# Kernel optimization log

Hardware: AMD Instinct MI355X
Metric: run time of the kernel (lower is better)

The kernel has to match this reference:

```python
import jax, jax.numpy as jnp
import numpy as np
from jax import lax

NUM_GROUP = 512
GROUP_SIZE = 32


def fps(xyz, npoint):
    """Farthest point sampling. xyz: [B, N, 3] -> centers [B, npoint, 3]."""
    B, N, _ = xyz.shape
    big = jnp.asarray(1e10, xyz.dtype)

    def body(carry, _):
        min_d, farthest = carry  # [B, N], [B]
        centroid = jnp.take_along_axis(xyz, farthest[:, None, None], axis=1)  # [B,1,3]
        d = jnp.sum((xyz - centroid) ** 2, axis=-1)  # [B, N]
        min_d = jnp.minimum(min_d, d)
        nxt = jnp.argmax(min_d, axis=-1).astype(jnp.int32)
        return (min_d, nxt), farthest

    init = (jnp.full((B, N), big, xyz.dtype), jnp.zeros((B,), jnp.int32))
    _, idxs = lax.scan(body, init, None, length=npoint)  # [npoint, B]
    idxs = idxs.T  # [B, npoint]
    return jnp.take_along_axis(xyz, idxs[..., None], axis=1)  # [B, npoint, 3]


def knn_idx(xyz, center, k):
    """xyz [B,N,3], center [B,G,3] -> idx [B,G,k] of k nearest (squared L2)."""
    # [B, G, N] squared distances
    d2 = jnp.sum((center[:, :, None, :] - xyz[:, None, :, :]) ** 2, axis=-1)
    _, idx = lax.top_k(-d2, k)  # smallest distances
    return idx


def setup_inputs() -> dict:
    key = jax.random.key(0)
    xyz = jax.random.normal(key, (32, 3, 8192), dtype=jnp.float32)
    return {"xyz": xyz}


def reference(xyz):
    # xyz: [B, 3, N] -> [B, N, 3]
    pts = jnp.transpose(xyz, (0, 2, 1))[:, :, :3]
    B, N, _ = pts.shape
    center = fps(pts, NUM_GROUP)                  # [B, G, 3]
    idx = knn_idx(pts, center, GROUP_SIZE)        # [B, G, k]
    flat_idx = idx.reshape(B, NUM_GROUP * GROUP_SIZE)
    neighborhood = jnp.take_along_axis(pts, flat_idx[..., None], axis=1)
    neighborhood = neighborhood.reshape(B, NUM_GROUP, GROUP_SIZE, 3)
    neighborhood = neighborhood - center[:, :, None, :]
    return neighborhood, center
```

## Files before the change

### kernel.cpp

```cpp
#include <hip/hip_runtime.h>

typedef unsigned long long u64;
typedef unsigned int u32;
typedef float v2f __attribute__((ext_vector_type(2)));

#define BATCH 32
#define NPTS  8192
#define NGRP  512
#define KNN_K 32

#define FPS_T 256
#define FPS_W (FPS_T / 64)
#define PPAIR (NPTS / FPS_T / 2)

#define KNN_WPB 8
#define KNN_T   (KNN_WPB * 64)
#define QCAP    128

#define NCH     (NPTS / 64)
#define GC      16
#define NCELL   (GC * GC * GC)
#define QB      512
#define BT      512
#define BPT     (NPTS / BT)
#define WSF     (4 * NPTS + NCH * 6)

__device__ __forceinline__ float sq3(float dx, float dy, float dz) {
    return __fadd_rn(__fadd_rn(__fmul_rn(dx, dx), __fmul_rn(dy, dy)), __fmul_rn(dz, dz));
}

__device__ __forceinline__ u64 packdi(float d, int n) {
    return ((u64)__float_as_uint(d) << 32) | (u32)n;
}

__device__ __forceinline__ u64 umin64(u64 a, u64 b) { return a < b ? a : b; }
__device__ __forceinline__ u64 umax64(u64 a, u64 b) { return a > b ? a : b; }

__device__ __forceinline__ u64 shfl_xor_u64(u64 v, int m) {
    int lo = __shfl_xor((int)(u32)v, m, 64);
    int hi = __shfl_xor((int)(u32)(v >> 32), m, 64);
    return ((u64)(u32)hi << 32) | (u32)lo;
}

__device__ __forceinline__ u64 shfl_u64(u64 v, int src) {
    int lo = __shfl((int)(u32)v, src, 64);
    int hi = __shfl((int)(u32)(v >> 32), src, 64);
    return ((u64)(u32)hi << 32) | (u32)lo;
}

template <int CTRL>
__device__ __forceinline__ u64 dpp_max_step(u64 k) {
    u32 plo = (u32)__builtin_amdgcn_update_dpp(0, (int)(u32)k, CTRL, 0xF, 0xF, true);
    u32 phi = (u32)__builtin_amdgcn_update_dpp(0, (int)(u32)(k >> 32), CTRL, 0xF, 0xF, true);
    u64 p = ((u64)phi << 32) | plo;
    return k > p ? k : p;
}
__device__ __forceinline__ u64 dpp_wave_max(u64 k) {
    k = dpp_max_step<0x111>(k);
    k = dpp_max_step<0x112>(k);
    k = dpp_max_step<0x114>(k);
    k = dpp_max_step<0x118>(k);
    k = dpp_max_step<0x142>(k);
    k = dpp_max_step<0x143>(k);
    return k;
}

__device__ __forceinline__ u64 lane_sort64(u64 v, int lane) {
#pragma unroll
    for (int k = 2; k <= 64; k <<= 1) {
#pragma unroll
        for (int j = k >> 1; j > 0; j >>= 1) {
            u64 p = shfl_xor_u64(v, j);
            bool keepmin = (((lane & k) == 0) == ((lane & j) == 0));
            u64 mn = umin64(v, p), mx = umax64(v, p);
            v = keepmin ? mn : mx;
        }
    }
    return v;
}

__device__ __forceinline__ u64 lane_merge64(u64 m, u64 c, int lane) {
    u64 cr = shfl_xor_u64(c, 63);
    u64 z = umin64(m, cr);
#pragma unroll
    for (int dd = 32; dd > 0; dd >>= 1) {
        u64 p = shfl_xor_u64(z, dd);
        u64 mn = umin64(z, p), mx = umax64(z, p);
        z = (lane & dd) ? mx : mn;
    }
    return z;
}

__device__ __forceinline__ void knn_step(u64& m, u64& tau, int& cnt, u64* sbuf,
                                         float x, float y, float z,
                                         float cx, float cy, float cz,
                                         int n, int lane) {
    float d = sq3(__fsub_rn(x, cx), __fsub_rn(y, cy), __fsub_rn(z, cz));
    u64 kk = packdi(d, n);
    bool cand = kk < tau;
    u64 mask = __ballot(cand);
    if (mask) {
        u32 below = __builtin_amdgcn_mbcnt_hi(
            (u32)(mask >> 32), __builtin_amdgcn_mbcnt_lo((u32)mask, 0));
        if (cand) sbuf[cnt + below] = kk;
        cnt += (int)__popcll(mask);
        if (cnt >= 64) {
            u64 c = sbuf[lane];
            c = lane_sort64(c, lane);
            m = lane_merge64(m, c, lane);
            tau = shfl_u64(m, 31);
            int rem = cnt - 64;
            if (lane < rem) sbuf[lane] = sbuf[64 + lane];
            cnt = rem;
        }
    }
}

__global__ __launch_bounds__(FPS_T) void fps_kernel(const float* __restrict__ in,
                                                    float* __restrict__ centers) {
#pragma clang fp contract(off)
    __shared__ float sx[NPTS];
    __shared__ float sy[NPTS];
    __shared__ float sz[NPTS];
    __shared__ u64 s_key[2][FPS_W];
    __shared__ float s_out[NGRP * 3];

    const int b = blockIdx.x;
    const int t = threadIdx.x;
    const int w = t >> 6;
    const float* xp = in + (size_t)b * 3 * NPTS;
    const float* yp = xp + NPTS;
    const float* zp = xp + 2 * NPTS;

    v2f xr[PPAIR], yr[PPAIR], zr[PPAIR], md[PPAIR];
#pragma unroll
    for (int i = 0; i < PPAIR; ++i) {
        int n = i * (2 * FPS_T) + 2 * t;
        xr[i] = *(const v2f*)(xp + n);
        yr[i] = *(const v2f*)(yp + n);
        zr[i] = *(const v2f*)(zp + n);
        *(v2f*)(sx + n) = xr[i];
        *(v2f*)(sy + n) = yr[i];
        *(v2f*)(sz + n) = zr[i];
        md[i] = (v2f){1e10f, 1e10f};
    }
    __syncthreads();

    int cur = 0;
    for (int r = 0; r < NGRP; ++r) {
        const float cx = sx[cur], cy = sy[cur], cz = sz[cur];
        if (t == 0) {
            s_out[r * 3 + 0] = cx;
            s_out[r * 3 + 1] = cy;
            s_out[r * 3 + 2] = cz;
        }

        float bd0 = -1.0f, bd1 = -1.0f;
        int   bi0 = 0,     bi1 = 0;
#pragma unroll
        for (int i = 0; i < PPAIR; ++i) {
            v2f dx = xr[i] - cx;
            v2f dy = yr[i] - cy;
            v2f dz = zr[i] - cz;
            v2f dd = dx * dx + dy * dy + dz * dz;
            md[i] = __builtin_elementwise_min(md[i], dd);
            int n = i * (2 * FPS_T) + 2 * t;
            if (md[i].x > bd0) { bd0 = md[i].x; bi0 = n; }
            if (md[i].y > bd1) { bd1 = md[i].y; bi1 = n + 1; }
        }
        u64 k0 = ((u64)__float_as_uint(bd0) << 32) | (u32)(~(u32)bi0);
        u64 k1 = ((u64)__float_as_uint(bd1) << 32) | (u32)(~(u32)bi1);
        u64 k = dpp_wave_max(umax64(k0, k1));
        if ((t & 63) == 63) s_key[r & 1][w] = k;
        __syncthreads();
        u64 m = umax64(umax64(s_key[r & 1][0], s_key[r & 1][1]),
                       umax64(s_key[r & 1][2], s_key[r & 1][3]));
        cur = (int)(~(u32)m);
    }

    __syncthreads();
    float* cdst = centers + (size_t)b * NGRP * 3;
    for (int i = t; i < NGRP * 3; i += FPS_T) cdst[i] = s_out[i];
}

__device__ __forceinline__ int qbin(float v) {
    int c = (int)((v + 4.0f) * 64.0f);
    c = c < 0 ? 0 : c;
    return c > (QB - 1) ? (QB - 1) : c;
}
__device__ __forceinline__ u32 part3_4(u32 v) {
    return (v & 1u) | ((v & 2u) << 2) | ((v & 4u) << 4) | ((v & 8u) << 6);
}

__global__ __launch_bounds__(BT) void build_kernel(const float* __restrict__ in,
                                                   float* __restrict__ ws) {
    __shared__ u32 hist[NCELL];
    __shared__ u32 hq[3][QB];
    __shared__ float sxl[NPTS];
    __shared__ float syl[NPTS];
    __shared__ float szl[NPTS];
    __shared__ u32 wtot[3][BT / 64];

    const int b = blockIdx.x;
    const int t = threadIdx.x;
    const int lane = t & 63;
    const int w = t >> 6;
    const float* xp = in + (size_t)b * 3 * NPTS;
    const float* yp = xp + NPTS;
    const float* zp = xp + 2 * NPTS;
    float* wsb = ws + (size_t)b * WSF;
    float* ws_sx = wsb;
    float* ws_sy = wsb + NPTS;
    float* ws_sz = wsb + 2 * NPTS;
    u32*   ws_si = (u32*)(wsb + 3 * NPTS);
    float* ws_ab = wsb + 4 * NPTS;

    for (int i = t; i < NCELL; i += BT) hist[i] = 0;
    for (int i = t; i < 3 * QB; i += BT) (&hq[0][0])[i] = 0;
    __syncthreads();

    float px[BPT], py[BPT], pz[BPT];
#pragma unroll
    for (int i = 0; i < BPT; ++i) {
        int n = i * BT + t;
        px[i] = xp[n]; py[i] = yp[n]; pz[i] = zp[n];
        atomicAdd(&hq[0][qbin(px[i])], 1u);
        atomicAdd(&hq[1][qbin(py[i])], 1u);
        atomicAdd(&hq[2][qbin(pz[i])], 1u);
    }
    __syncthreads();

    {
        u32 v0 = hq[0][t], v1 = hq[1][t], v2 = hq[2][t];
        u32 x0 = v0, x1 = v1, x2 = v2;
#pragma unroll
        for (int d = 1; d < 64; d <<= 1) {
            u32 y0 = __shfl_up(x0, d, 64), y1 = __shfl_up(x1, d, 64), y2 = __shfl_up(x2, d, 64);
            if (lane >= d) { x0 += y0; x1 += y1; x2 += y2; }
        }
        if (lane == 63) { wtot[0][w] = x0; wtot[1][w] = x1; wtot[2][w] = x2; }
        __syncthreads();
        u32 b0 = 0, b1 = 0, b2 = 0;
        for (int j = 0; j < w; ++j) { b0 += wtot[0][j]; b1 += wtot[1][j]; b2 += wtot[2][j]; }
        hq[0][t] = (b0 + x0 - v0) >> 9;
        hq[1][t] = (b1 + x1 - v1) >> 9;
        hq[2][t] = (b2 + x2 - v2) >> 9;
    }
    __syncthreads();

    int pc[BPT];
#pragma unroll
    for (int i = 0; i < BPT; ++i) {
        u32 cxq = hq[0][qbin(px[i])];
        u32 cyq = hq[1][qbin(py[i])];
        u32 czq = hq[2][qbin(pz[i])];
        pc[i] = (int)(part3_4(cxq) | (part3_4(cyq) << 1) | (part3_4(czq) << 2));
        atomicAdd(&hist[pc[i]], 1u);
    }
    __syncthreads();

    u32 h[NCELL / BT];
    u32 lsum = 0;
#pragma unroll
    for (int j = 0; j < NCELL / BT; ++j) { h[j] = hist[t * (NCELL / BT) + j]; lsum += h[j]; }
    u32 x = lsum;
#pragma unroll
    for (int d = 1; d < 64; d <<= 1) {
        u32 y = __shfl_up(x, d, 64);
        if (lane >= d) x += y;
    }
    if (lane == 63) wtot[0][w] = x;
    u32 wexcl = x - lsum;
    __syncthreads();
    u32 base = 0;
    for (int j = 0; j < w; ++j) base += wtot[0][j];
    u32 run = base + wexcl;
#pragma unroll
    for (int j = 0; j < NCELL / BT; ++j) {
        u32 c = h[j];
        hist[t * (NCELL / BT) + j] = run;
        run += c;
    }
    __syncthreads();

#pragma unroll
    for (int i = 0; i < BPT; ++i) {
        u32 pos = atomicAdd(&hist[pc[i]], 1u);
        sxl[pos] = px[i]; syl[pos] = py[i]; szl[pos] = pz[i];
        ws_si[pos] = (u32)(i * BT + t);
    }
    __syncthreads();

    for (int i = t; i < NPTS; i += BT) {
        ws_sx[i] = sxl[i]; ws_sy[i] = syl[i]; ws_sz[i] = szl[i];
    }
    for (int q = w; q < NCH; q += BT / 64) {
        int p = q * 64 + lane;
        float X = sxl[p], Y = syl[p], Z = szl[p];
        float xlo = X, xhi = X, ylo = Y, yhi = Y, zlo = Z, zhi = Z;
#pragma unroll
        for (int d = 1; d < 64; d <<= 1) {
            xlo = fminf(xlo, __shfl_xor(xlo, d, 64)); xhi = fmaxf(xhi, __shfl_xor(xhi, d, 64));
            ylo = fminf(ylo, __shfl_xor(ylo, d, 64)); yhi = fmaxf(yhi, __shfl_xor(yhi, d, 64));
            zlo = fminf(zlo, __shfl_xor(zlo, d, 64)); zhi = fmaxf(zhi, __shfl_xor(zhi, d, 64));
        }
        if (lane == 0) {
            float* a = ws_ab + q * 6;
            a[0] = xlo; a[1] = xhi; a[2] = ylo; a[3] = yhi; a[4] = zlo; a[5] = zhi;
        }
    }
}

__global__ __launch_bounds__(KNN_T) void knn_kernel(const float* __restrict__ in,
                                                    const float* __restrict__ centers,
                                                    const float* __restrict__ ws,
                                                    float* __restrict__ out) {
    __shared__ float s_ab[NCH * 6];
    __shared__ u64 sbuf[KNN_WPB][QCAP];

    const int wave = threadIdx.x >> 6;
    const int lane = threadIdx.x & 63;
    const int cid  = blockIdx.x * KNN_WPB + wave;
    const int b    = cid >> 9;

    const float* xp = in + (size_t)b * 3 * NPTS;
    const float* yp = xp + NPTS;
    const float* zp = xp + 2 * NPTS;
    const float* wsb = ws + (size_t)b * WSF;
    const float* sxs = wsb;
    const float* sys = wsb + NPTS;
    const float* szs = wsb + 2 * NPTS;
    const u32*   sidx = (const u32*)(wsb + 3 * NPTS);
    const float* ab = wsb + 4 * NPTS;

    for (int i = threadIdx.x; i < NCH * 6; i += KNN_T) s_ab[i] = ab[i];
    __syncthreads();

    const float cx = centers[cid * 3 + 0];
    const float cy = centers[cid * 3 + 1];
    const float cz = centers[cid * 3 + 2];

    u64 k0, k1;
    {
        const float* a0 = &s_ab[lane * 6];
        float dx = fmaxf(fmaxf(__fsub_rn(a0[0], cx), __fsub_rn(cx, a0[1])), 0.0f);
        float dy = fmaxf(fmaxf(__fsub_rn(a0[2], cy), __fsub_rn(cy, a0[3])), 0.0f);
        float dz = fmaxf(fmaxf(__fsub_rn(a0[4], cz), __fsub_rn(cz, a0[5])), 0.0f);
        k0 = ((u64)__float_as_uint(dx * dx + dy * dy + dz * dz) << 32) | (u32)lane;
        const float* a1 = &s_ab[(lane + 64) * 6];
        dx = fmaxf(fmaxf(__fsub_rn(a1[0], cx), __fsub_rn(cx, a1[1])), 0.0f);
        dy = fmaxf(fmaxf(__fsub_rn(a1[2], cy), __fsub_rn(cy, a1[3])), 0.0f);
        dz = fmaxf(fmaxf(__fsub_rn(a1[4], cz), __fsub_rn(cz, a1[5])), 0.0f);
        k1 = ((u64)__float_as_uint(dx * dx + dy * dy + dz * dz) << 32) | (u32)(lane + 64);
    }

    u64 m, tau;
    int cnt = 0;

    {
        u64 inv = dpp_wave_max(~umin64(k0, k1));
        u64 got = ~shfl_u64(inv, 63);
        int c = (int)(u32)got;
        int p = c * 64 + lane;
        float X = sxs[p], Y = sys[p], Z = szs[p];
        int n = (int)sidx[p];
        m = lane_sort64(packdi(sq3(__fsub_rn(X, cx), __fsub_rn(Y, cy), __fsub_rn(Z, cz)), n),
                        lane);
        tau = shfl_u64(m, 31);
        if (lane == (c & 63)) { if (c < 64) k0 = ~0ull; else k1 = ~0ull; }
    }

    for (int it = 1; it < NCH; ++it) {
        u64 inv = dpp_wave_max(~umin64(k0, k1));
        u64 got = ~shfl_u64(inv, 63);
        float lb = __uint_as_float((u32)(got >> 32));
        float tau_d = __uint_as_float((u32)(tau >> 32));
        if (lb * 0.999f > tau_d) break;
        int c = (int)(u32)got;
        int p = c * 64 + lane;
        float X = sxs[p], Y = sys[p], Z = szs[p];
        int n = (int)sidx[p];
        knn_step(m, tau, cnt, sbuf[wave], X, Y, Z, cx, cy, cz, n, lane);
        if (lane == (c & 63)) { if (c < 64) k0 = ~0ull; else k1 = ~0ull; }
    }

    while (cnt > 0) {
        int take = cnt < 64 ? cnt : 64;
        u64 v = sbuf[wave][lane];
        u64 c = (lane < take) ? v : ~0ull;
        c = lane_sort64(c, lane);
        m = lane_merge64(m, c, lane);
        int rem = cnt - take;
        if (lane < rem) sbuf[wave][lane] = sbuf[wave][64 + lane];
        cnt = rem;
    }

    if (lane < KNN_K) {
        int n = (int)(u32)m;
        size_t o = (size_t)cid * (KNN_K * 3) + (size_t)lane * 3;
        out[o + 0] = __fsub_rn(xp[n], cx);
        out[o + 1] = __fsub_rn(yp[n], cy);
        out[o + 2] = __fsub_rn(zp[n], cz);
    }
}

#define KNN_WPB_FB 4
__global__ __launch_bounds__(KNN_WPB_FB * 64) void knn_fallback(
    const float* __restrict__ in, const float* __restrict__ centers,
    float* __restrict__ out) {
    __shared__ u64 sbuf[KNN_WPB_FB][QCAP];

    const int wave = threadIdx.x >> 6;
    const int lane = threadIdx.x & 63;
    const int cid  = blockIdx.x * KNN_WPB_FB + wave;
    const int b    = cid >> 9;

    const float* xp = in + (size_t)b * 3 * NPTS;
    const float* yp = xp + NPTS;
    const float* zp = xp + 2 * NPTS;

    const float cx = centers[cid * 3 + 0];
    const float cy = centers[cid * 3 + 1];
    const float cz = centers[cid * 3 + 2];

    float x = xp[lane], y = yp[lane], z = zp[lane];
    u64 m = packdi(sq3(__fsub_rn(x, cx), __fsub_rn(y, cy), __fsub_rn(z, cz)), lane);
    m = lane_sort64(m, lane);
    u64 tau = shfl_u64(m, 31);
    int cnt = 0;

    int j = 1;
#pragma unroll 1
    for (; j + 3 < NPTS / 64; j += 4) {
        int n0 = j * 64 + lane, n1 = n0 + 64, n2 = n0 + 128, n3 = n0 + 192;
        float x0 = xp[n0], y0 = yp[n0], z0 = zp[n0];
        float x1 = xp[n1], y1 = yp[n1], z1 = zp[n1];
        float x2 = xp[n2], y2 = yp[n2], z2 = zp[n2];
        float x3 = xp[n3], y3 = yp[n3], z3 = zp[n3];
        knn_step(m, tau, cnt, sbuf[wave], x0, y0, z0, cx, cy, cz, n0, lane);
        knn_step(m, tau, cnt, sbuf[wave], x1, y1, z1, cx, cy, cz, n1, lane);
        knn_step(m, tau, cnt, sbuf[wave], x2, y2, z2, cx, cy, cz, n2, lane);
        knn_step(m, tau, cnt, sbuf[wave], x3, y3, z3, cx, cy, cz, n3, lane);
    }
    for (; j < NPTS / 64; ++j) {
        int n = j * 64 + lane;
        knn_step(m, tau, cnt, sbuf[wave], xp[n], yp[n], zp[n], cx, cy, cz, n, lane);
    }
    while (cnt > 0) {
        int take = cnt < 64 ? cnt : 64;
        u64 v = sbuf[wave][lane];
        u64 c = (lane < take) ? v : ~0ull;
        c = lane_sort64(c, lane);
        m = lane_merge64(m, c, lane);
        int rem = cnt - take;
        if (lane < rem) sbuf[wave][lane] = sbuf[wave][64 + lane];
        cnt = rem;
    }
    if (lane < KNN_K) {
        int n = (int)(u32)m;
        size_t o = (size_t)cid * (KNN_K * 3) + (size_t)lane * 3;
        out[o + 0] = __fsub_rn(xp[n], cx);
        out[o + 1] = __fsub_rn(yp[n], cy);
        out[o + 2] = __fsub_rn(zp[n], cz);
    }
}

extern "C" void kernel_launch(void* const* d_in, const int* in_sizes, int n_in,
                              void* d_out, int out_size, void* d_ws, size_t ws_size,
                              hipStream_t stream) {
    const float* in  = (const float*)d_in[0];
    float* out       = (float*)d_out;
    float* centers   = out + (size_t)BATCH * NGRP * KNN_K * 3;

    const size_t need = (size_t)BATCH * WSF * sizeof(float);

    fps_kernel<<<BATCH, FPS_T, 0, stream>>>(in, centers);
    if (d_ws != nullptr && ws_size >= need) {
        build_kernel<<<BATCH, BT, 0, stream>>>(in, (float*)d_ws);
        knn_kernel<<<(BATCH * NGRP) / KNN_WPB, KNN_T, 0, stream>>>(
            in, centers, (const float*)d_ws, out);
    } else {
        knn_fallback<<<(BATCH * NGRP) / KNN_WPB_FB, KNN_WPB_FB * 64, 0, stream>>>(
            in, centers, out);
    }
}
```

Before: 555.5 us.

## Run FPS on spatially sorted points with per-thread bounding-box pruning

Adds an FPS kernel that reads the grid-sorted point layout produced by the build kernel, so each thread owns 32 spatially contiguous points, and computes their bounding box. Each round the thread skips its distance update when the box's lower-bound distance to the new centroid cannot lower its cached maximum min-distance, and reuses its cached key instead. Ties are broken on original indices kept in shared memory, so the result matches the reference argmax. Exchange: an extra u16 index array in LDS, a dependency on build_kernel before FPS (which removes FPS/build overlap), and warp divergence when only some threads skip.

```diff
diff --git a/kernel.cpp b/kernel.cpp
--- a/kernel.cpp
+++ b/kernel.cpp
@@ -2,6 +2,7 @@
 
 typedef unsigned long long u64;
 typedef unsigned int u32;
+typedef unsigned short u16;
 typedef float v2f __attribute__((ext_vector_type(2)));
 
 #define BATCH 32
@@ -116,6 +117,107 @@
     }
 }
 
+__global__ __launch_bounds__(FPS_T) void fps_sorted_kernel(const float* __restrict__ in,
+                                                           const float* __restrict__ ws,
+                                                           float* __restrict__ centers) {
+#pragma clang fp contract(off)
+    __shared__ float sx[NPTS];
+    __shared__ float sy[NPTS];
+    __shared__ float sz[NPTS];
+    __shared__ u16 s_orig[NPTS];
+    __shared__ u64 s_key[2][FPS_W];
+    __shared__ float s_out[NGRP * 3];
+
+    const int b = blockIdx.x;
+    const int t = threadIdx.x;
+    const int w = t >> 6;
+    const float* xp = in + (size_t)b * 3 * NPTS;
+    const float* wsb = ws + (size_t)b * WSF;
+    const float* sxs = wsb;
+    const float* sys = wsb + NPTS;
+    const float* szs = wsb + 2 * NPTS;
+    const u32*   sidx = (const u32*)(wsb + 3 * NPTS);
+
+    for (int i = t; i < NPTS; i += FPS_T) {
+        sx[i] = sxs[i]; sy[i] = sys[i]; sz[i] = szs[i];
+        s_orig[i] = (u16)sidx[i];
+    }
+
+    const int base = t * 32;
+    v2f xr[PPAIR], yr[PPAIR], zr[PPAIR], md[PPAIR];
+    float axlo = 1e30f, axhi = -1e30f, aylo = 1e30f, ayhi = -1e30f,
+          azlo = 1e30f, azhi = -1e30f;
+#pragma unroll
+    for (int i = 0; i < PPAIR; ++i) {
+        xr[i] = *(const v2f*)(sxs + base + 2 * i);
+        yr[i] = *(const v2f*)(sys + base + 2 * i);
+        zr[i] = *(const v2f*)(szs + base + 2 * i);
+        md[i] = (v2f){1e10f, 1e10f};
+        axlo = fminf(axlo, fminf(xr[i].x, xr[i].y)); axhi = fmaxf(axhi, fmaxf(xr[i].x, xr[i].y));
+        aylo = fminf(aylo, fminf(yr[i].x, yr[i].y)); ayhi = fmaxf(ayhi, fmaxf(yr[i].x, yr[i].y));
+        azlo = fminf(azlo, fminf(zr[i].x, zr[i].y)); azhi = fmaxf(azhi, fmaxf(zr[i].x, zr[i].y));
+    }
+    __syncthreads();
+
+    float cxv = xp[0], cyv = xp[NPTS], czv = xp[2 * NPTS];
+    float ub = 1e10f;
+    u64 kcache = 0;
+
+    for (int r = 0; r < NGRP; ++r) {
+        if (t == 0) {
+            s_out[r * 3 + 0] = cxv;
+            s_out[r * 3 + 1] = cyv;
+            s_out[r * 3 + 2] = czv;
+        }
+
+        float dxl = fmaxf(fmaxf(axlo - cxv, cxv - axhi), 0.0f);
+        float dyl = fmaxf(fmaxf(aylo - cyv, cyv - ayhi), 0.0f);
+        float dzl = fmaxf(fmaxf(azlo - czv, czv - azhi), 0.0f);
+        float lb = dxl * dxl + dyl * dyl + dzl * dzl;
+
+        u64 k;
+        if (__fmul_rn(lb, 0.99f) <= ub) {
+            float bd0 = -1.0f, bd1 = -1.0f;
+            int   bs0 = base,  bs1 = base;
+#pragma unroll
+            for (int i = 0; i < PPAIR; ++i) {
+                v2f dx = xr[i] - cxv;
+                v2f dy = yr[i] - cyv;
+                v2f dz = zr[i] - czv;
+                v2f dd = dx * dx + dy * dy + dz * dz;
+                md[i] = __builtin_elementwise_min(md[i], dd);
+                int sp = base + 2 * i;
+                if (md[i].x > bd0) { bd0 = md[i].x; bs0 = sp; }
+                else if (md[i].x == bd0 && s_orig[sp] < s_orig[bs0]) bs0 = sp;
+                if (md[i].y > bd1) { bd1 = md[i].y; bs1 = sp + 1; }
+                else if (md[i].y == bd1 && s_orig[sp + 1] < s_orig[bs1]) bs1 = sp + 1;
+            }
+            u32 o0 = s_orig[bs0], o1 = s_orig[bs1];
+            u64 kk0 = ((u64)__float_as_uint(bd0) << 32) |
+                      ((u64)(8191u - o0) << 13) | (u32)bs0;
+            u64 kk1 = ((u64)__float_as_uint(bd1) << 32) |
+                      ((u64)(8191u - o1) << 13) | (u32)bs1;
+            k = umax64(kk0, kk1);
+            ub = fmaxf(bd0, bd1);
+            kcache = k;
+        } else {
+            k = kcache;
+        }
+
+        k = dpp_wave_max(k);
+        if ((t & 63) == 63) s_key[r & 1][w] = k;
+        __syncthreads();
+        u64 m = umax64(umax64(s_key[r & 1][0], s_key[r & 1][1]),
+                       umax64(s_key[r & 1][2], s_key[r & 1][3]));
+        int spos = (int)(m & 0x1FFFull);
+        cxv = sx[spos]; cyv = sy[spos]; czv = sz[spos];
+    }
+
+    __syncthreads();
+    float* cdst = centers + (size_t)b * NGRP * 3;
+    for (int i = t; i < NGRP * 3; i += FPS_T) cdst[i] = s_out[i];
+}
+
 __global__ __launch_bounds__(FPS_T) void fps_kernel(const float* __restrict__ in,
                                                     float* __restrict__ centers) {
 #pragma clang fp contract(off)
@@ -474,12 +576,13 @@
 
     const size_t need = (size_t)BATCH * WSF * sizeof(float);
 
-    fps_kernel<<<BATCH, FPS_T, 0, stream>>>(in, centers);
     if (d_ws != nullptr && ws_size >= need) {
         build_kernel<<<BATCH, BT, 0, stream>>>(in, (float*)d_ws);
+        fps_sorted_kernel<<<BATCH, FPS_T, 0, stream>>>(in, (const float*)d_ws, centers);
         knn_kernel<<<(BATCH * NGRP) / KNN_WPB, KNN_T, 0, stream>>>(
             in, centers, (const float*)d_ws, out);
     } else {
+        fps_kernel<<<BATCH, FPS_T, 0, stream>>>(in, centers);
         knn_fallback<<<(BATCH * NGRP) / KNN_WPB_FB, KNN_WPB_FB * 64, 0, stream>>>(
             in, centers, out);
     }
```

After: 1.510 ms. 2.72x slower.

## Fuse FPS and KNN into one persistent kernel with flag-based streaming of centers

Applied to the files above, without the earlier changes.

FPS and KNN now run inside one launch. The first BATCH blocks run FPS and publish each new center to global memory, then bump a per-batch progress flag with release semantics. The remaining blocks spin on that flag with acquire loads and run the KNN search for a center as soon as it is available. This overlaps the serial FPS loop with the KNN work and removes the separate launch, but it relies on all blocks being co-resident, adds spin-waiting, and uses only 7 KNN blocks per batch.

```diff
diff --git a/kernel.cpp b/kernel.cpp
--- a/kernel.cpp
+++ b/kernel.cpp
@@ -13,13 +13,15 @@
 #define FPS_W (FPS_T / 64)
 #define PPAIR (NPTS / FPS_T / 2)
 
+#define FUSED_T 512
 #define KNN_WPB 8
-#define KNN_T   (KNN_WPB * 64)
 #define QCAP    128
+#define NKB     7
+#define KGRID   (BATCH * NKB)
+#define NWAVE_B (NKB * 8)
 
 #define NCH     (NPTS / 64)
-#define GC      16
-#define NCELL   (GC * GC * GC)
+#define NCELL   (16 * 16 * 16)
 #define QB      512
 #define BT      512
 #define BPT     (NPTS / BT)
@@ -116,71 +118,209 @@
     }
 }
 
-__global__ __launch_bounds__(FPS_T) void fps_kernel(const float* __restrict__ in,
-                                                    float* __restrict__ centers) {
+struct FpsS {
+    float sx[NPTS]; float sy[NPTS]; float sz[NPTS];
+    u64 s_key[2][FPS_W];
+};
+struct KnnS {
+    float s_ab[NCH * 6];
+    u64 sbuf[KNN_WPB][QCAP];
+};
+
+__global__ __launch_bounds__(FUSED_T) void fused_kernel(const float* __restrict__ in,
+                                                        const float* __restrict__ ws,
+                                                        u32* __restrict__ flags,
+                                                        float* __restrict__ centers,
+                                                        float* __restrict__ out) {
 #pragma clang fp contract(off)
-    __shared__ float sx[NPTS];
-    __shared__ float sy[NPTS];
-    __shared__ float sz[NPTS];
-    __shared__ u64 s_key[2][FPS_W];
-    __shared__ float s_out[NGRP * 3];
-
-    const int b = blockIdx.x;
-    const int t = threadIdx.x;
-    const int w = t >> 6;
+    __shared__ alignas(16) char smem_raw[sizeof(FpsS)];
+
+    if (blockIdx.x < BATCH) {
+        FpsS& S = *reinterpret_cast<FpsS*>(smem_raw);
+        const int b = blockIdx.x;
+        const int t = threadIdx.x;
+        const float* xp = in + (size_t)b * 3 * NPTS;
+        const float* yp = xp + NPTS;
+        const float* zp = xp + 2 * NPTS;
+        u32* cball = (u32*)(centers + (size_t)b * NGRP * 3);
+
+        v2f xr[PPAIR], yr[PPAIR], zr[PPAIR], md[PPAIR];
+        if (t < FPS_T) {
+#pragma unroll
+            for (int i = 0; i < PPAIR; ++i) {
+                int n = i * (2 * FPS_T) + 2 * t;
+                xr[i] = *(const v2f*)(xp + n);
+                yr[i] = *(const v2f*)(yp + n);
+                zr[i] = *(const v2f*)(zp + n);
+                *(v2f*)(S.sx + n) = xr[i];
+                *(v2f*)(S.sy + n) = yr[i];
+                *(v2f*)(S.sz + n) = zr[i];
+                md[i] = (v2f){1e10f, 1e10f};
+            }
+        }
+        __syncthreads();
+
+        if (t == FPS_T) {
+            __hip_atomic_store(cball + 0, __float_as_uint(xp[0]),
+                               __ATOMIC_RELAXED, __HIP_MEMORY_SCOPE_AGENT);
+            __hip_atomic_store(cball + 1, __float_as_uint(yp[0]),
+                               __ATOMIC_RELAXED, __HIP_MEMORY_SCOPE_AGENT);
+            __hip_atomic_store(cball + 2, __float_as_uint(zp[0]),
+                               __ATOMIC_RELAXED, __HIP_MEMORY_SCOPE_AGENT);
+            __hip_atomic_store(&flags[b], 1u,
+                               __ATOMIC_RELEASE, __HIP_MEMORY_SCOPE_AGENT);
+        }
+
+        int cur = 0;
+        const int w = t >> 6;
+        for (int r = 0; r < NGRP - 1; ++r) {
+            if (t < FPS_T) {
+                const float cx = S.sx[cur], cy = S.sy[cur], cz = S.sz[cur];
+                float bd0 = -1.0f, bd1 = -1.0f;
+                int   bi0 = 0,     bi1 = 0;
+#pragma unroll
+                for (int i = 0; i < PPAIR; ++i) {
+                    v2f dx = xr[i] - cx;
+                    v2f dy = yr[i] - cy;
+                    v2f dz = zr[i] - cz;
+                    v2f dd = dx * dx + dy * dy + dz * dz;
+                    md[i] = __builtin_elementwise_min(md[i], dd);
+                    int n = i * (2 * FPS_T) + 2 * t;
+                    if (md[i].x > bd0) { bd0 = md[i].x; bi0 = n; }
+                    if (md[i].y > bd1) { bd1 = md[i].y; bi1 = n + 1; }
+                }
+                u64 k0 = ((u64)__float_as_uint(bd0) << 32) | (u32)(~(u32)bi0);
+                u64 k1 = ((u64)__float_as_uint(bd1) << 32) | (u32)(~(u32)bi1);
+                u64 k = dpp_wave_max(umax64(k0, k1));
+                if ((t & 63) == 63) S.s_key[r & 1][w] = k;
+            }
+            __syncthreads();
+            if (t < FPS_T) {
+                u64 m = umax64(umax64(S.s_key[r & 1][0], S.s_key[r & 1][1]),
+                               umax64(S.s_key[r & 1][2], S.s_key[r & 1][3]));
+                cur = (int)(~(u32)m);
+            } else if (t == FPS_T) {
+                u64 m = umax64(umax64(S.s_key[r & 1][0], S.s_key[r & 1][1]),
+                               umax64(S.s_key[r & 1][2], S.s_key[r & 1][3]));
+                int win = (int)(~(u32)m);
+                u32* cd = cball + (size_t)(r + 1) * 3;
+                __hip_atomic_store(cd + 0, __float_as_uint(S.sx[win]),
+                                   __ATOMIC_RELAXED, __HIP_MEMORY_SCOPE_AGENT);
+                __hip_atomic_store(cd + 1, __float_as_uint(S.sy[win]),
+                                   __ATOMIC_RELAXED, __HIP_MEMORY_SCOPE_AGENT);
+                __hip_atomic_store(cd + 2, __float_as_uint(S.sz[win]),
+                                   __ATOMIC_RELAXED, __HIP_MEMORY_SCOPE_AGENT);
+                __hip_atomic_store(&flags[b], (u32)(r + 2),
+                                   __ATOMIC_RELEASE, __HIP_MEMORY_SCOPE_AGENT);
+            }
+        }
+        return;
+    }
+
+    KnnS& S = *reinterpret_cast<KnnS*>(smem_raw);
+    const int kb   = blockIdx.x - BATCH;
+    const int b    = kb / NKB;
+    const int sub  = kb % NKB;
+    const int wave = threadIdx.x >> 6;
+    const int lane = threadIdx.x & 63;
+
     const float* xp = in + (size_t)b * 3 * NPTS;
     const float* yp = xp + NPTS;
     const float* zp = xp + 2 * NPTS;
-
-    v2f xr[PPAIR], yr[PPAIR], zr[PPAIR], md[PPAIR];
-#pragma unroll
-    for (int i = 0; i < PPAIR; ++i) {
-        int n = i * (2 * FPS_T) + 2 * t;
-        xr[i] = *(const v2f*)(xp + n);
-        yr[i] = *(const v2f*)(yp + n);
-        zr[i] = *(const v2f*)(zp + n);
-        *(v2f*)(sx + n) = xr[i];
-        *(v2f*)(sy + n) = yr[i];
-        *(v2f*)(sz + n) = zr[i];
-        md[i] = (v2f){1e10f, 1e10f};
-    }
-    __syncthreads();
-
-    int cur = 0;
-    for (int r = 0; r < NGRP; ++r) {
-        const float cx = sx[cur], cy = sy[cur], cz = sz[cur];
-        if (t == 0) {
-            s_out[r * 3 + 0] = cx;
-            s_out[r * 3 + 1] = cy;
-            s_out[r * 3 + 2] = cz;
-        }
-
-        float bd0 = -1.0f, bd1 = -1.0f;
-        int   bi0 = 0,     bi1 = 0;
-#pragma unroll
-        for (int i = 0; i < PPAIR; ++i) {
-            v2f dx = xr[i] - cx;
-            v2f dy = yr[i] - cy;
-            v2f dz = zr[i] - cz;
-            v2f dd = dx * dx + dy * dy + dz * dz;
-            md[i] = __builtin_elementwise_min(md[i], dd);
-            int n = i * (2 * FPS_T) + 2 * t;
-            if (md[i].x > bd0) { bd0 = md[i].x; bi0 = n; }
-            if (md[i].y > bd1) { bd1 = md[i].y; bi1 = n + 1; }
-        }
-        u64 k0 = ((u64)__float_as_uint(bd0) << 32) | (u32)(~(u32)bi0);
-        u64 k1 = ((u64)__float_as_uint(bd1) << 32) | (u32)(~(u32)bi1);
-        u64 k = dpp_wave_max(umax64(k0, k1));
-        if ((t & 63) == 63) s_key[r & 1][w] = k;
-        __syncthreads();
-        u64 m = umax64(umax64(s_key[r & 1][0], s_key[r & 1][1]),
-                       umax64(s_key[r & 1][2], s_key[r & 1][3]));
-        cur = (int)(~(u32)m);
-    }
-
-    __syncthreads();
-    float* cdst = centers + (size_t)b * NGRP * 3;
-    for (int i = t; i < NGRP * 3; i += FPS_T) cdst[i] = s_out[i];
+    const float* wsb = ws + (size_t)b * WSF;
+    const float* sxs = wsb;
+    const float* sys = wsb + NPTS;
+    const float* szs = wsb + 2 * NPTS;
+    const u32*   sidx = (const u32*)(wsb + 3 * NPTS);
+    const float* ab = wsb + 4 * NPTS;
+    const u32* cball = (const u32*)(centers + (size_t)b * NGRP * 3);
+
+    for (int i = threadIdx.x; i < NCH * 6; i += FUSED_T) S.s_ab[i] = ab[i];
+    __syncthreads();
+
+    const int wg = sub * 8 + wave;
+    for (int g = wg; g < NGRP; g += NWAVE_B) {
+        float cxl = 0.f, cyl = 0.f, czl = 0.f;
+        if (lane == 0) {
+            while (__hip_atomic_load(&flags[b], __ATOMIC_ACQUIRE,
+                                     __HIP_MEMORY_SCOPE_AGENT) <= (u32)g)
+                __builtin_amdgcn_s_sleep(8);
+            const u32* cs = cball + (size_t)g * 3;
+            cxl = __uint_as_float(__hip_atomic_load(cs + 0, __ATOMIC_RELAXED,
+                                                    __HIP_MEMORY_SCOPE_AGENT));
+            cyl = __uint_as_float(__hip_atomic_load(cs + 1, __ATOMIC_RELAXED,
+                                                    __HIP_MEMORY_SCOPE_AGENT));
+            czl = __uint_as_float(__hip_atomic_load(cs + 2, __ATOMIC_RELAXED,
+                                                    __HIP_MEMORY_SCOPE_AGENT));
+        }
+        const float cx = __shfl(cxl, 0, 64);
+        const float cy = __shfl(cyl, 0, 64);
+        const float cz = __shfl(czl, 0, 64);
+        const int cid = (b << 9) + g;
+
+        u64 k0, k1;
+        {
+            const float* a0 = &S.s_ab[lane * 6];
+            float dx = fmaxf(fmaxf(__fsub_rn(a0[0], cx), __fsub_rn(cx, a0[1])), 0.0f);
+            float dy = fmaxf(fmaxf(__fsub_rn(a0[2], cy), __fsub_rn(cy, a0[3])), 0.0f);
+            float dz = fmaxf(fmaxf(__fsub_rn(a0[4], cz), __fsub_rn(cz, a0[5])), 0.0f);
+            k0 = ((u64)__float_as_uint(dx * dx + dy * dy + dz * dz) << 32) | (u32)lane;
+            const float* a1 = &S.s_ab[(lane + 64) * 6];
+            dx = fmaxf(fmaxf(__fsub_rn(a1[0], cx), __fsub_rn(cx, a1[1])), 0.0f);
+            dy = fmaxf(fmaxf(__fsub_rn(a1[2], cy), __fsub_rn(cy, a1[3])), 0.0f);
+            dz = fmaxf(fmaxf(__fsub_rn(a1[4], cz), __fsub_rn(cz, a1[5])), 0.0f);
+            k1 = ((u64)__float_as_uint(dx * dx + dy * dy + dz * dz) << 32) | (u32)(lane + 64);
+        }
+
+        u64 m, tau;
+        int cnt = 0;
+
+        {
+            u64 inv = dpp_wave_max(~umin64(k0, k1));
+            u64 got = ~shfl_u64(inv, 63);
+            int c = (int)(u32)got;
+            int p = c * 64 + lane;
+            float X = sxs[p], Y = sys[p], Z = szs[p];
+            int n = (int)sidx[p];
+            m = lane_sort64(packdi(sq3(__fsub_rn(X, cx), __fsub_rn(Y, cy),
+                                       __fsub_rn(Z, cz)), n), lane);
+            tau = shfl_u64(m, 31);
+            if (lane == (c & 63)) { if (c < 64) k0 = ~0ull; else k1 = ~0ull; }
+        }
+
+        for (int it = 1; it < NCH; ++it) {
+            u64 inv = dpp_wave_max(~umin64(k0, k1));
+            u64 got = ~shfl_u64(inv, 63);
+            float lb = __uint_as_float((u32)(got >> 32));
+            float tau_d = __uint_as_float((u32)(tau >> 32));
+            if (lb * 0.999f > tau_d) break;
+            int c = (int)(u32)got;
+            int p = c * 64 + lane;
+            float X = sxs[p], Y = sys[p], Z = szs[p];
+            int n = (int)sidx[p];
+            knn_step(m, tau, cnt, S.sbuf[wave], X, Y, Z, cx, cy, cz, n, lane);
+            if (lane == (c & 63)) { if (c < 64) k0 = ~0ull; else k1 = ~0ull; }
+        }
+
+        while (cnt > 0) {
+            int take = cnt < 64 ? cnt : 64;
+            u64 v = S.sbuf[wave][lane];
+            u64 c = (lane < take) ? v : ~0ull;
+            c = lane_sort64(c, lane);
+            m = lane_merge64(m, c, lane);
+            int rem = cnt - take;
+            if (lane < rem) S.sbuf[wave][lane] = S.sbuf[wave][64 + lane];
+            cnt = rem;
+        }
+
+        if (lane < KNN_K) {
+            int n = (int)(u32)m;
+            size_t o = (size_t)cid * (KNN_K * 3) + (size_t)lane * 3;
+            out[o + 0] = __fsub_rn(xp[n], cx);
+            out[o + 1] = __fsub_rn(yp[n], cy);
+            out[o + 2] = __fsub_rn(zp[n], cz);
+        }
+    }
 }
 
 __device__ __forceinline__ int qbin(float v) {
@@ -215,6 +355,11 @@
     u32*   ws_si = (u32*)(wsb + 3 * NPTS);
     float* ws_ab = wsb + 4 * NPTS;
 
+    if (t == 0) {
+        u32* fl = (u32*)(ws + (size_t)BATCH * WSF);
+        __hip_atomic_store(&fl[b], 0u, __ATOMIC_RELAXED, __HIP_MEMORY_SCOPE_AGENT);
+    }
+
     for (int i = t; i < NCELL; i += BT) hist[i] = 0;
     for (int i = t; i < 3 * QB; i += BT) (&hq[0][0])[i] = 0;
     __syncthreads();
@@ -311,97 +456,70 @@
     }
 }
 
-__global__ __launch_bounds__(KNN_T) void knn_kernel(const float* __restrict__ in,
-                                                    const float* __restrict__ centers,
-                                                    const float* __restrict__ ws,
-                                                    float* __restrict__ out) {
-    __shared__ float s_ab[NCH * 6];
-    __shared__ u64 sbuf[KNN_WPB][QCAP];
-
-    const int wave = threadIdx.x >> 6;
-    const int lane = threadIdx.x & 63;
-    const int cid  = blockIdx.x * KNN_WPB + wave;
-    const int b    = cid >> 9;
-
+__global__ __launch_bounds__(FPS_T) void fps_kernel(const float* __restrict__ in,
+                                                    float* __restrict__ centers) {
+#pragma clang fp contract(off)
+    __shared__ float sx[NPTS];
+    __shared__ float sy[NPTS];
+    __shared__ float sz[NPTS];
+    __shared__ u64 s_key[2][FPS_W];
+    __shared__ float s_out[NGRP * 3];
+
+    const int b = blockIdx.x;
+    const int t = threadIdx.x;
+    const int w = t >> 6;
     const float* xp = in + (size_t)b * 3 * NPTS;
     const float* yp = xp + NPTS;
     const float* zp = xp + 2 * NPTS;
-    const float* wsb = ws + (size_t)b * WSF;
-    const float* sxs = wsb;
-    const float* sys = wsb + NPTS;
-    const float* szs = wsb + 2 * NPTS;
-    const u32*   sidx = (const u32*)(wsb + 3 * NPTS);
-    const float* ab = wsb + 4 * NPTS;
-
-    for (int i = threadIdx.x; i < NCH * 6; i += KNN_T) s_ab[i] = ab[i];
-    __syncthreads();
-
-    const float cx = centers[cid * 3 + 0];
-    const float cy = centers[cid * 3 + 1];
-    const float cz = centers[cid * 3 + 2];
-
-    u64 k0, k1;
-    {
-        const float* a0 = &s_ab[lane * 6];
-        float dx = fmaxf(fmaxf(__fsub_rn(a0[0], cx), __fsub_rn(cx, a0[1])), 0.0f);
-        float dy = fmaxf(fmaxf(__fsub_rn(a0[2], cy), __fsub_rn(cy, a0[3])), 0.0f);
-        float dz = fmaxf(fmaxf(__fsub_rn(a0[4], cz), __fsub_rn(cz, a0[5])), 0.0f);
-        k0 = ((u64)__float_as_uint(dx * dx + dy * dy + dz * dz) << 32) | (u32)lane;
-        const float* a1 = &s_ab[(lane + 64) * 6];
-        dx = fmaxf(fmaxf(__fsub_rn(a1[0], cx), __fsub_rn(cx, a1[1])), 0.0f);
-        dy = fmaxf(fmaxf(__fsub_rn(a1[2], cy), __fsub_rn(cy, a1[3])), 0.0f);
-        dz = fmaxf(fmaxf(__fsub_rn(a1[4], cz), __fsub_rn(cz, a1[5])), 0.0f);
-        k1 = ((u64)__float_as_uint(dx * dx + dy * dy + dz * dz) << 32) | (u32)(lane + 64);
-    }
-
-    u64 m, tau;
-    int cnt = 0;
-
-    {
-        u64 inv = dpp_wave_max(~umin64(k0, k1));
-        u64 got = ~shfl_u64(inv, 63);
-        int c = (int)(u32)got;
-        int p = c * 64 + lane;
-        float X = sxs[p], Y = sys[p], Z = szs[p];
-        int n = (int)sidx[p];
-        m = lane_sort64(packdi(sq3(__fsub_rn(X, cx), __fsub_rn(Y, cy), __fsub_rn(Z, cz)), n),
-                        lane);
-        tau = shfl_u64(m, 31);
-        if (lane == (c & 63)) { if (c < 64) k0 = ~0ull; else k1 = ~0ull; }
-    }
-
-    for (int it = 1; it < NCH; ++it) {
-        u64 inv = dpp_wave_max(~umin64(k0, k1));
-        u64 got = ~shfl_u64(inv, 63);
-        float lb = __uint_as_float((u32)(got >> 32));
-        float tau_d = __uint_as_float((u32)(tau >> 32));
-        if (lb * 0.999f > tau_d) break;
-        int c = (int)(u32)got;
-        int p = c * 64 + lane;
-        float X = sxs[p], Y = sys[p], Z = szs[p];
-        int n = (int)sidx[p];
-        knn_step(m, tau, cnt, sbuf[wave], X, Y, Z, cx, cy, cz, n, lane);
-        if (lane == (c & 63)) { if (c < 64) k0 = ~0ull; else k1 = ~0ull; }
-    }
-
-    while (cnt > 0) {
-        int take = cnt < 64 ? cnt : 64;
-        u64 v = sbuf[wave][lane];
-        u64 c = (lane < take) ? v : ~0ull;
-        c = lane_sort64(c, lane);
-        m = lane_merge64(m, c, lane);
-        int rem = cnt - take;
-        if (lane < rem) sbuf[wave][lane] = sbuf[wave][64 + lane];
-        cnt = rem;
-    }
-
-    if (lane < KNN_K) {
-        int n = (int)(u32)m;
-        size_t o = (size_t)cid * (KNN_K * 3) + (size_t)lane * 3;
-        out[o + 0] = __fsub_rn(xp[n], cx);
-        out[o + 1] = __fsub_rn(yp[n], cy);
-        out[o + 2] = __fsub_rn(zp[n], cz);
-    }
+
+    v2f xr[PPAIR], yr[PPAIR], zr[PPAIR], md[PPAIR];
+#pragma unroll
+    for (int i = 0; i < PPAIR; ++i) {
+        int n = i * (2 * FPS_T) + 2 * t;
+        xr[i] = *(const v2f*)(xp + n);
+        yr[i] = *(const v2f*)(yp + n);
+        zr[i] = *(const v2f*)(zp + n);
+        *(v2f*)(sx + n) = xr[i];
+        *(v2f*)(sy + n) = yr[i];
+        *(v2f*)(sz + n) = zr[i];
+        md[i] = (v2f){1e10f, 1e10f};
+    }
+    __syncthreads();
+
+    int cur = 0;
+    for (int r = 0; r < NGRP; ++r) {
+        const float cx = sx[cur], cy = sy[cur], cz = sz[cur];
+        if (t == 0) {
+            s_out[r * 3 + 0] = cx;
+            s_out[r * 3 + 1] = cy;
+            s_out[r * 3 + 2] = cz;
+        }
+        float bd0 = -1.0f, bd1 = -1.0f;
+        int   bi0 = 0,     bi1 = 0;
+#pragma unroll
+        for (int i = 0; i < PPAIR; ++i) {
+            v2f dx = xr[i] - cx;
+            v2f dy = yr[i] - cy;
+            v2f dz = zr[i] - cz;
+            v2f dd = dx * dx + dy * dy + dz * dz;
+            md[i] = __builtin_elementwise_min(md[i], dd);
+            int n = i * (2 * FPS_T) + 2 * t;
+            if (md[i].x > bd0) { bd0 = md[i].x; bi0 = n; }
+            if (md[i].y > bd1) { bd1 = md[i].y; bi1 = n + 1; }
+        }
+        u64 k0 = ((u64)__float_as_uint(bd0) << 32) | (u32)(~(u32)bi0);
+        u64 k1 = ((u64)__float_as_uint(bd1) << 32) | (u32)(~(u32)bi1);
+        u64 k = dpp_wave_max(umax64(k0, k1));
+        if ((t & 63) == 63) s_key[r & 1][w] = k;
+        __syncthreads();
+        u64 m = umax64(umax64(s_key[r & 1][0], s_key[r & 1][1]),
+                       umax64(s_key[r & 1][2], s_key[r & 1][3]));
+        cur = (int)(~(u32)m);
+    }
+
+    __syncthreads();
+    float* cdst = centers + (size_t)b * NGRP * 3;
+    for (int i = t; i < NGRP * 3; i += FPS_T) cdst[i] = s_out[i];
 }
 
 #define KNN_WPB_FB 4
@@ -472,14 +590,15 @@
     float* out       = (float*)d_out;
     float* centers   = out + (size_t)BATCH * NGRP * KNN_K * 3;
 
-    const size_t need = (size_t)BATCH * WSF * sizeof(float);
-
-    fps_kernel<<<BATCH, FPS_T, 0, stream>>>(in, centers);
+    const size_t need = ((size_t)BATCH * WSF + BATCH) * sizeof(float);
+
     if (d_ws != nullptr && ws_size >= need) {
-        build_kernel<<<BATCH, BT, 0, stream>>>(in, (float*)d_ws);
-        knn_kernel<<<(BATCH * NGRP) / KNN_WPB, KNN_T, 0, stream>>>(
-            in, centers, (const float*)d_ws, out);
+        float* ws = (float*)d_ws;
+        u32* flags = (u32*)(ws + (size_t)BATCH * WSF);
+        build_kernel<<<BATCH, BT, 0, stream>>>(in, ws);
+        fused_kernel<<<BATCH + KGRID, FUSED_T, 0, stream>>>(in, ws, flags, centers, out);
     } else {
+        fps_kernel<<<BATCH, FPS_T, 0, stream>>>(in, centers);
         knn_fallback<<<(BATCH * NGRP) / KNN_WPB_FB, KNN_WPB_FB * 64, 0, stream>>>(
             in, centers, out);
     }
```

Result: slower. 2.080 ms (+274.5%).
